# Optimization experiments

Measured on AMD Instinct MI355X. Metric: run time of the kernel, lower is better.

## Reference

```python
import jax, jax.numpy as jnp
import numpy as np

# Concrete instantiation of MACE MessagePassingConvolution for
# node irreps = 128x0e + 128x1o, target irreps = 128x0e + 128x1o, max_ell = 2.
# With these irreps the e3nn tensor product keeps exactly these paths:
#   0e (x) Y1o -> 1o ,  1o (x) Y1o -> 0e ,  1o (x) Y2e -> 1o
# plus the filtered original 0e and 1o features. Normalization constants are
# named below (stand-ins for e3nn's CG / component normalization).

C = 128                      # channels per irrep
AVG_NUM_NEIGHBORS = 10.0
SH_L1 = np.sqrt(3.0)         # component-normalized Y_1 scale
SH_L2 = np.sqrt(7.5)         # component-normalized Y_2 scale
CG_011 = 1.0 / np.sqrt(3.0)  # 0e x 1o -> 1o path norm
CG_110 = 1.0 / np.sqrt(3.0)  # 1o x 1o -> 0e path norm
CG_121 = np.sqrt(0.4)        # 1o x 2e -> 1o path norm


def setup_inputs() -> dict:
    key = jax.random.key(0)
    ks = jax.random.split(key, 9)
    N, E, R = 10000, 100000, 8
    return {
        "vectors": jax.random.normal(ks[0], (E, 3), jnp.float32),
        "node_feats": jax.random.normal(ks[1], (N, C + 3 * C), jnp.float32),
        "radial_embedding": jax.random.normal(ks[2], (E, R), jnp.float32),
        "w0": jax.random.normal(ks[3], (R, 64), jnp.float32),
        "w1": jax.random.normal(ks[4], (64, 64), jnp.float32),
        "w2": jax.random.normal(ks[5], (64, 64), jnp.float32),
        "w3": jax.random.normal(ks[6], (64, 5 * C), jnp.float32),
        "senders": jax.random.randint(ks[7], (E,), 0, N, jnp.int32),
        "receivers": jax.random.randint(ks[8], (E,), 0, N, jnp.int32),
    }


def reference(vectors, node_feats, radial_embedding, w0, w1, w2, w3, senders, receivers):
    N = node_feats.shape[0]
    s = node_feats[:, :C]                         # [N,C]   0e scalars
    v = node_feats[:, C:].reshape(N, C, 3)        # [N,C,3] 1o vectors

    # gather sender features onto edges
    ss = s[senders]                               # [E,C]
    vs = v[senders]                               # [E,C,3]

    # spherical harmonics of edge vectors (normalized input, per e3nn)
    rn = vectors / jnp.linalg.norm(vectors, axis=-1, keepdims=True)   # [E,3]
    Y1 = SH_L1 * rn                                                   # [E,3]  l=1
    Y2 = SH_L2 * (rn[:, :, None] * rn[:, None, :] - jnp.eye(3, dtype=rn.dtype) / 3.0)  # [E,3,3] l=2 (traceless sym)

    # tensor product paths filtered to target irreps 0e + 1o
    tp1 = CG_011 * ss[:, :, None] * Y1[:, None, :]            # [E,C,3]  0e x 1o -> 1o
    tp0 = CG_110 * jnp.einsum('eci,ei->ec', vs, Y1)           # [E,C]    1o x 1o -> 0e
    tp2 = CG_121 * jnp.einsum('eij,ecj->eci', Y2, vs)         # [E,C,3]  1o x 2e -> 1o

    # regrouped messages: scalars then vectors
    msg_s = jnp.concatenate([ss, tp0], axis=1)                # [E,2C]
    msg_v = jnp.concatenate([vs, tp1, tp2], axis=1)           # [E,3C,3]

    # radial MLP gating (e3nn-style normalized linears: x @ W / sqrt(fan_in))
    h = radial_embedding
    for W in (w0, w1, w2):
        h = jax.nn.silu(h @ W / jnp.sqrt(jnp.asarray(W.shape[0], h.dtype)))
    mix = h @ w3 / jnp.sqrt(jnp.asarray(w3.shape[0], h.dtype))        # [E,5C]

    msg_s = msg_s * mix[:, : 2 * C]
    msg_v = msg_v * mix[:, 2 * C :, None]

    # scatter-add into receivers, normalize by sqrt(avg_num_neighbors)
    out_s = jax.ops.segment_sum(msg_s, receivers, num_segments=N)     # [N,2C]
    out_v = jax.ops.segment_sum(msg_v, receivers, num_segments=N)     # [N,3C,3]
    out = jnp.concatenate([out_s, out_v.reshape(N, -1)], axis=1)      # [N,11C]
    return out / jnp.sqrt(jnp.asarray(AVG_NUM_NEIGHBORS, out.dtype))
```

## Files before the change

kernel.cpp:

```cpp
#include <hip/hip_runtime.h>

#define CCH   128
#define NF    512
#define OUTF  1408
#define RDIM  8

#define INV_SQRT8  0.35355339059327373f
#define INV_SQRT10 0.31622776601683794f
#define SQRT3      1.7320508075688772f

typedef _Float16 half2_t __attribute__((ext_vector_type(2)));

__device__ __forceinline__ float silu(float x) {
    return x / (1.0f + __expf(-x));
}

__device__ __forceinline__ unsigned int packh2(float lo, float hi) {
    half2_t h = { (_Float16)lo, (_Float16)hi };
    return __builtin_bit_cast(unsigned int, h);
}
__device__ __forceinline__ float h2lo(unsigned int u) {
    return (float)__builtin_bit_cast(half2_t, u).x;
}
__device__ __forceinline__ float h2hi(unsigned int u) {
    return (float)__builtin_bit_cast(half2_t, u).y;
}

__device__ __forceinline__ float dot2(unsigned int h, unsigned int w, float c) {
#if __has_builtin(__builtin_amdgcn_fdot2)
    return __builtin_amdgcn_fdot2(__builtin_bit_cast(half2_t, h),
                                  __builtin_bit_cast(half2_t, w), c, false);
#else
    half2_t a = __builtin_bit_cast(half2_t, h);
    half2_t b = __builtin_bit_cast(half2_t, w);
    return c + (float)a.x * (float)b.x + (float)a.y * (float)b.y;
#endif
}

__global__ void k_zero(int* __restrict__ p, int n) {
    int i = blockIdx.x * 256 + threadIdx.x;
    if (i < n) p[i] = 0;
}

__global__ void k_hist(const int* __restrict__ recv, int* __restrict__ counts, int E) {
    int i = blockIdx.x * 256 + threadIdx.x;
    if (i < E) atomicAdd(&counts[recv[i]], 1);
}

__global__ void k_scan(const int* __restrict__ counts, int* __restrict__ offsets,
                       int* __restrict__ cursor, int n) {
    __shared__ int wsum[16];
    int t = threadIdx.x;
    int lane = t & 63, wid = t >> 6;
    int carry = 0;
    for (int base = 0; base < n; base += 1024) {
        int i = base + t;
        int x = (i < n) ? counts[i] : 0;
        int s = x;
        #pragma unroll
        for (int off = 1; off < 64; off <<= 1) {
            int v = __shfl_up(s, off, 64);
            if (lane >= off) s += v;
        }
        if (lane == 63) wsum[wid] = s;
        __syncthreads();
        if (wid == 0) {
            int v = (lane < 16) ? wsum[lane] : 0;
            #pragma unroll
            for (int off = 1; off < 16; off <<= 1) {
                int u = __shfl_up(v, off, 64);
                if (lane >= off) v += u;
            }
            if (lane < 16) wsum[lane] = v;
        }
        __syncthreads();
        int excl_wave = (wid > 0) ? wsum[wid - 1] : 0;
        int incl = s + excl_wave;
        if (i < n) {
            int ex = carry + incl - x;
            offsets[i] = ex;
            cursor[i]  = ex;
        }
        carry += wsum[15];
        __syncthreads();
    }
    if (t == 0) offsets[n] = carry;
}

__global__ void k_perm(const int* __restrict__ recv, int* __restrict__ cursor,
                       int* __restrict__ perm, int E) {
    int i = blockIdx.x * 256 + threadIdx.x;
    if (i < E) {
        int p = atomicAdd(&cursor[recv[i]], 1);
        perm[p] = i;
    }
}

__global__ __launch_bounds__(256, 4) void k_mlp2(
    const float* __restrict__ radial,
    const float* __restrict__ w0, const float* __restrict__ w1,
    const float* __restrict__ w2, _Float16* __restrict__ h2out, int E)
{
    __shared__ float        w0s[8 * 64];
    __shared__ unsigned int w1p[32 * 64];
    __shared__ unsigned int w2p[32 * 64];
    __shared__ _Float16     hs[4][4][64];

    for (int idx = threadIdx.x; idx < 512; idx += 256) w0s[idx] = w0[idx];
    for (int idx = threadIdx.x; idx < 2048; idx += 256) {
        int j = idx & 63, kp = idx >> 6;
        w1p[idx] = packh2(w1[(2 * kp) * 64 + j], w1[(2 * kp + 1) * 64 + j]);
        w2p[idx] = packh2(w2[(2 * kp) * 64 + j], w2[(2 * kp + 1) * 64 + j]);
    }
    __syncthreads();

    const int lane = threadIdx.x & 63;
    const int wid  = threadIdx.x >> 6;
    unsigned int* hsu = (unsigned int*)&hs[wid][0][0];

    int e0 = (blockIdx.x * 4 + wid) * 4;

    float w0r[8];
    #pragma unroll
    for (int k = 0; k < 8; k++) w0r[k] = w0s[k * 64 + lane];
    #pragma unroll
    for (int q = 0; q < 4; q++) {
        int e = e0 + q; if (e >= E) e = E - 1;
        const float* r = radial + (size_t)e * RDIM;
        float acc = 0.f;
        #pragma unroll
        for (int k = 0; k < 8; k++) acc += r[k] * w0r[k];
        hs[wid][q][lane] = (_Float16)silu(acc * INV_SQRT8);
    }
    __syncthreads();

    float acc1[4] = {0.f, 0.f, 0.f, 0.f};
    #pragma unroll 4
    for (int kp = 0; kp < 32; kp++) {
        unsigned int w = w1p[kp * 64 + lane];
        #pragma unroll
        for (int q = 0; q < 4; q++) acc1[q] = dot2(hsu[q * 32 + kp], w, acc1[q]);
    }
    __syncthreads();
    #pragma unroll
    for (int q = 0; q < 4; q++) hs[wid][q][lane] = (_Float16)silu(acc1[q] * 0.125f);
    __syncthreads();

    float acc2[4] = {0.f, 0.f, 0.f, 0.f};
    #pragma unroll 4
    for (int kp = 0; kp < 32; kp++) {
        unsigned int w = w2p[kp * 64 + lane];
        #pragma unroll
        for (int q = 0; q < 4; q++) acc2[q] = dot2(hsu[q * 32 + kp], w, acc2[q]);
    }
    #pragma unroll
    for (int q = 0; q < 4; q++) {
        int e = e0 + q;
        if (e < E) h2out[(size_t)e * 64 + lane] = (_Float16)silu(acc2[q] * 0.125f);
    }
}

__global__ __launch_bounds__(512, 4) void k_mix(
    const float* __restrict__ w3,
    const unsigned int* __restrict__ h2g,
    unsigned int* __restrict__ mixp, int E)
{
    __shared__ uint4 wA[32 * 64];
    __shared__ uint4 wB[32 * 64];
    __shared__ uint2 wC[32 * 64];

    for (int idx = threadIdx.x; idx < 32 * 64; idx += 512) {
        int lane = idx & 63, kp = idx >> 6;
        const float* r0 = w3 + (2 * kp) * 640;
        const float* r1 = r0 + 640;
        uint4 A, B; uint2 Cc;
        A.x = packh2(r0[lane],       r1[lane]);
        A.y = packh2(r0[lane + 64],  r1[lane + 64]);
        A.z = packh2(r0[lane + 128], r1[lane + 128]);
        A.w = packh2(r0[lane + 192], r1[lane + 192]);
        B.x = packh2(r0[lane + 256], r1[lane + 256]);
        B.y = packh2(r0[lane + 320], r1[lane + 320]);
        B.z = packh2(r0[lane + 384], r1[lane + 384]);
        B.w = packh2(r0[lane + 448], r1[lane + 448]);
        Cc.x = packh2(r0[lane + 512], r1[lane + 512]);
        Cc.y = packh2(r0[lane + 576], r1[lane + 576]);
        wA[idx] = A; wB[idx] = B; wC[idx] = Cc;
    }
    __syncthreads();

    const int lane = threadIdx.x & 63;
    int wave = blockIdx.x * 8 + (threadIdx.x >> 6);
    int nwaves = gridDim.x * 8;
    int nquads = (E + 3) >> 2;
    const float sc = 0.125f * INV_SQRT10;

    for (int t = wave; t < nquads; t += nwaves) {
        int e0 = t * 4;
        const unsigned int* hp[4];
        #pragma unroll
        for (int q = 0; q < 4; q++) {
            int e = e0 + q; if (e >= E) e = E - 1;
            hp[q] = h2g + (size_t)e * 32;
        }

        float mixv[4][10];
        #pragma unroll
        for (int q = 0; q < 4; q++)
            #pragma unroll
            for (int m = 0; m < 10; m++) mixv[q][m] = 0.f;

        #pragma unroll 4
        for (int kp = 0; kp < 32; kp++) {
            unsigned int hq[4];
            #pragma unroll
            for (int q = 0; q < 4; q++) hq[q] = hp[q][kp];
            uint4 A  = wA[kp * 64 + lane];
            uint4 B  = wB[kp * 64 + lane];
            uint2 Cc = wC[kp * 64 + lane];
            #pragma unroll
            for (int q = 0; q < 4; q++) {
                unsigned int h = hq[q];
                mixv[q][0] = dot2(h, A.x,  mixv[q][0]);
                mixv[q][1] = dot2(h, A.y,  mixv[q][1]);
                mixv[q][2] = dot2(h, A.z,  mixv[q][2]);
                mixv[q][3] = dot2(h, A.w,  mixv[q][3]);
                mixv[q][4] = dot2(h, B.x,  mixv[q][4]);
                mixv[q][5] = dot2(h, B.y,  mixv[q][5]);
                mixv[q][6] = dot2(h, B.z,  mixv[q][6]);
                mixv[q][7] = dot2(h, B.w,  mixv[q][7]);
                mixv[q][8] = dot2(h, Cc.x, mixv[q][8]);
                mixv[q][9] = dot2(h, Cc.y, mixv[q][9]);
            }
        }

        #pragma unroll
        for (int q = 0; q < 4; q++) {
            int e = e0 + q;
            if (e < E) {
                unsigned int* mp = mixp + (size_t)e * 320 + lane;
                mp[0]   = packh2(mixv[q][0] * sc,         mixv[q][1] * sc);
                mp[64]  = packh2(mixv[q][2] * sc,         mixv[q][3] * sc);
                mp[128] = packh2(mixv[q][4] * sc,         mixv[q][5] * sc);
                mp[192] = packh2(mixv[q][6] * sc,         mixv[q][7] * sc);
                mp[256] = packh2(mixv[q][8] * sc * SQRT3, mixv[q][9] * sc * SQRT3);
            }
        }
    }
}

__global__ __launch_bounds__(256, 4) void k_gather(
    const float* __restrict__ vectors,
    const float* __restrict__ node_feats,
    const int*   __restrict__ senders,
    const int*   __restrict__ offsets,
    const int*   __restrict__ perm,
    const unsigned int* __restrict__ mixp,
    float* __restrict__ out, int N)
{
    const int lane = threadIdx.x & 63;
    int node = blockIdx.x * 4 + (threadIdx.x >> 6);
    if (node >= N) return;

    int beg = offsets[node];
    int end = offsets[node + 1];

    float aS[2]     = {0.f, 0.f};
    float aT0[2]    = {0.f, 0.f};
    float aV0[2][3] = {{0.f,0.f,0.f},{0.f,0.f,0.f}};
    float aV1[2][3] = {{0.f,0.f,0.f},{0.f,0.f,0.f}};
    float aV2[2][3] = {{0.f,0.f,0.f},{0.f,0.f,0.f}};

    for (int i = beg; i < end; i++) {
        int e = perm[i];
        float vx = vectors[(size_t)e * 3 + 0];
        float vy = vectors[(size_t)e * 3 + 1];
        float vz = vectors[(size_t)e * 3 + 2];
        float inv = rsqrtf(vx * vx + vy * vy + vz * vz);
        float rx = vx * inv, ry = vy * inv, rz = vz * inv;
        int snd = senders[e];

        const unsigned int* mp = mixp + (size_t)e * 320 + lane;
        unsigned int u0 = mp[0], u1 = mp[64], u2 = mp[128], u3 = mp[192], u4 = mp[256];

        const float* nf = node_feats + (size_t)snd * NF;
        #pragma unroll
        for (int t = 0; t < 2; t++) {
            int c = lane + 64 * t;
            float ssv = nf[c];
            float v0 = nf[CCH + 3 * c + 0];
            float v1 = nf[CCH + 3 * c + 1];
            float v2 = nf[CCH + 3 * c + 2];
            float d = rx * v0 + ry * v1 + rz * v2;

            float m0 = t ? h2hi(u0) : h2lo(u0);
            float m1 = t ? h2hi(u1) : h2lo(u1);
            float m2 = t ? h2hi(u2) : h2lo(u2);
            float m3 = t ? h2hi(u3) : h2lo(u3);
            float m4 = t ? h2hi(u4) : h2lo(u4);

            aS[t]  += ssv * m0;
            aT0[t] += d * m1;
            aV0[t][0] += v0 * m2;
            aV0[t][1] += v1 * m2;
            aV0[t][2] += v2 * m2;
            aV1[t][0] += ssv * rx * m3;
            aV1[t][1] += ssv * ry * m3;
            aV1[t][2] += ssv * rz * m3;
            aV2[t][0] += (d * rx - v0 * (1.f / 3.f)) * m4;
            aV2[t][1] += (d * ry - v1 * (1.f / 3.f)) * m4;
            aV2[t][2] += (d * rz - v2 * (1.f / 3.f)) * m4;
        }
    }

    float* ob = out + (size_t)node * OUTF;
    #pragma unroll
    for (int t = 0; t < 2; t++) {
        int c = lane + 64 * t;
        ob[c]                = aS[t];
        ob[CCH + c]          = aT0[t];
        ob[256  + 3 * c + 0] = aV0[t][0];
        ob[256  + 3 * c + 1] = aV0[t][1];
        ob[256  + 3 * c + 2] = aV0[t][2];
        ob[640  + 3 * c + 0] = aV1[t][0];
        ob[640  + 3 * c + 1] = aV1[t][1];
        ob[640  + 3 * c + 2] = aV1[t][2];
        ob[1024 + 3 * c + 0] = aV2[t][0];
        ob[1024 + 3 * c + 1] = aV2[t][1];
        ob[1024 + 3 * c + 2] = aV2[t][2];
    }
}

__global__ __launch_bounds__(512, 4) void k_main_fused(
    const float* __restrict__ vectors,
    const float* __restrict__ node_feats,
    const float* __restrict__ w3,
    const int*   __restrict__ senders,
    const int*   __restrict__ offsets,
    const int*   __restrict__ perm,
    const unsigned int* __restrict__ h2g,
    int* __restrict__ ctr,
    float* __restrict__ out, int N)
{
    __shared__ uint4 wA[32 * 64];
    __shared__ uint4 wB[32 * 64];
    __shared__ uint2 wC[32 * 64];

    for (int idx = threadIdx.x; idx < 32 * 64; idx += 512) {
        int lane = idx & 63, kp = idx >> 6;
        const float* r0 = w3 + (2 * kp) * 640;
        const float* r1 = r0 + 640;
        uint4 A, B; uint2 Cc;
        A.x = packh2(r0[lane],       r1[lane]);
        A.y = packh2(r0[lane + 64],  r1[lane + 64]);
        A.z = packh2(r0[lane + 128], r1[lane + 128]);
        A.w = packh2(r0[lane + 192], r1[lane + 192]);
        B.x = packh2(r0[lane + 256], r1[lane + 256]);
        B.y = packh2(r0[lane + 320], r1[lane + 320]);
        B.z = packh2(r0[lane + 384], r1[lane + 384]);
        B.w = packh2(r0[lane + 448], r1[lane + 448]);
        Cc.x = packh2(r0[lane + 512], r1[lane + 512]);
        Cc.y = packh2(r0[lane + 576], r1[lane + 576]);
        wA[idx] = A; wB[idx] = B; wC[idx] = Cc;
    }
    __syncthreads();

    const int lane = threadIdx.x & 63;

    while (true) {
        int t0 = 0;
        if (lane == 0) t0 = atomicAdd(ctr, 1);
        int node = __shfl(t0, 0, 64);
        if (node >= N) break;
        node = __builtin_amdgcn_readfirstlane(node);

        int beg = offsets[node];
        int end = offsets[node + 1];

        float aS[2]     = {0.f, 0.f};
        float aT0[2]    = {0.f, 0.f};
        float aV0[2][3] = {{0.f,0.f,0.f},{0.f,0.f,0.f}};
        float aV1[2][3] = {{0.f,0.f,0.f},{0.f,0.f,0.f}};
        float aV2[2][3] = {{0.f,0.f,0.f},{0.f,0.f,0.f}};

        for (int i0 = beg; i0 < end; i0 += 4) {
            int rem = end - i0;
            int nq = rem < 4 ? rem : 4;

            const unsigned int* hrow[4];
            float rnx[4], rny[4], rnz[4];
            int   snd[4];

            #pragma unroll
            for (int q = 0; q < 4; q++) {
                int e = (q < nq) ? perm[i0 + q] : perm[i0];
                e = __builtin_amdgcn_readfirstlane(e);
                hrow[q] = h2g + (size_t)e * 32;
                if (q < nq) {
                    float vx = vectors[(size_t)e * 3 + 0];
                    float vy = vectors[(size_t)e * 3 + 1];
                    float vz = vectors[(size_t)e * 3 + 2];
                    float inv = rsqrtf(vx * vx + vy * vy + vz * vz);
                    rnx[q] = vx * inv; rny[q] = vy * inv; rnz[q] = vz * inv;
                    snd[q] = senders[e];
                }
            }

            float mixv[4][10];
            #pragma unroll
            for (int q = 0; q < 4; q++)
                #pragma unroll
                for (int m = 0; m < 10; m++) mixv[q][m] = 0.f;

            #pragma unroll 4
            for (int kp = 0; kp < 32; kp++) {
                unsigned int hq[4];
                #pragma unroll
                for (int q = 0; q < 4; q++) hq[q] = hrow[q][kp];
                uint4 A  = wA[kp * 64 + lane];
                uint4 B  = wB[kp * 64 + lane];
                uint2 Cc = wC[kp * 64 + lane];
                #pragma unroll
                for (int q = 0; q < 4; q++) {
                    unsigned int h = hq[q];
                    mixv[q][0] = dot2(h, A.x,  mixv[q][0]);
                    mixv[q][1] = dot2(h, A.y,  mixv[q][1]);
                    mixv[q][2] = dot2(h, A.z,  mixv[q][2]);
                    mixv[q][3] = dot2(h, A.w,  mixv[q][3]);
                    mixv[q][4] = dot2(h, B.x,  mixv[q][4]);
                    mixv[q][5] = dot2(h, B.y,  mixv[q][5]);
                    mixv[q][6] = dot2(h, B.z,  mixv[q][6]);
                    mixv[q][7] = dot2(h, B.w,  mixv[q][7]);
                    mixv[q][8] = dot2(h, Cc.x, mixv[q][8]);
                    mixv[q][9] = dot2(h, Cc.y, mixv[q][9]);
                }
            }

            const float sc = 0.125f * INV_SQRT10;
            #pragma unroll
            for (int q = 0; q < 4; q++) {
                if (q < nq) {
                    const float* nf = node_feats + (size_t)snd[q] * NF;
                    #pragma unroll
                    for (int t = 0; t < 2; t++) {
                        int c = lane + 64 * t;
                        float ssv = nf[c];
                        float v0 = nf[CCH + 3 * c + 0];
                        float v1 = nf[CCH + 3 * c + 1];
                        float v2 = nf[CCH + 3 * c + 2];
                        float d = rnx[q] * v0 + rny[q] * v1 + rnz[q] * v2;

                        float m0 = mixv[q][t]     * sc;
                        float m1 = mixv[q][2 + t] * sc;
                        float m2 = mixv[q][4 + t] * sc;
                        float m3 = mixv[q][6 + t] * sc;
                        float m4 = mixv[q][8 + t] * sc * SQRT3;

                        aS[t]  += ssv * m0;
                        aT0[t] += d * m1;
                        aV0[t][0] += v0 * m2;
                        aV0[t][1] += v1 * m2;
                        aV0[t][2] += v2 * m2;
                        aV1[t][0] += ssv * rnx[q] * m3;
                        aV1[t][1] += ssv * rny[q] * m3;
                        aV1[t][2] += ssv * rnz[q] * m3;
                        aV2[t][0] += (d * rnx[q] - v0 * (1.f / 3.f)) * m4;
                        aV2[t][1] += (d * rny[q] - v1 * (1.f / 3.f)) * m4;
                        aV2[t][2] += (d * rnz[q] - v2 * (1.f / 3.f)) * m4;
                    }
                }
            }
        }

        float* ob = out + (size_t)node * OUTF;
        #pragma unroll
        for (int t = 0; t < 2; t++) {
            int c = lane + 64 * t;
            ob[c]                = aS[t];
            ob[CCH + c]          = aT0[t];
            ob[256  + 3 * c + 0] = aV0[t][0];
            ob[256  + 3 * c + 1] = aV0[t][1];
            ob[256  + 3 * c + 2] = aV0[t][2];
            ob[640  + 3 * c + 0] = aV1[t][0];
            ob[640  + 3 * c + 1] = aV1[t][1];
            ob[640  + 3 * c + 2] = aV1[t][2];
            ob[1024 + 3 * c + 0] = aV2[t][0];
            ob[1024 + 3 * c + 1] = aV2[t][1];
            ob[1024 + 3 * c + 2] = aV2[t][2];
        }
    }
}

extern "C" void kernel_launch(void* const* d_in, const int* in_sizes, int n_in,
                              void* d_out, int out_size, void* d_ws, size_t ws_size,
                              hipStream_t stream) {
    const float* vectors    = (const float*)d_in[0];
    const float* node_feats = (const float*)d_in[1];
    const float* radial     = (const float*)d_in[2];
    const float* w0         = (const float*)d_in[3];
    const float* w1         = (const float*)d_in[4];
    const float* w2         = (const float*)d_in[5];
    const float* w3         = (const float*)d_in[6];
    const int*   senders    = (const int*)d_in[7];
    const int*   receivers  = (const int*)d_in[8];

    int E = in_sizes[0] / 3;
    int N = in_sizes[1] / NF;

    size_t small_elems = (size_t)E * 32 + N + 1 + (N + 1) + N + E;
    size_t full_elems  = (size_t)E * 320 + small_elems;
    bool big = ws_size >= full_elems * 4;

    unsigned int* mixp = (unsigned int*)d_ws;
    unsigned int* h2u  = mixp + (big ? (size_t)E * 320 : 0);
    int* counts  = (int*)(h2u + (size_t)E * 32);
    int* ctr     = counts + N;
    int* offsets = ctr + 1;
    int* cursor  = offsets + N + 1;
    int* perm    = cursor + N;
    _Float16* h2f = (_Float16*)h2u;

    k_zero<<<(N + 1 + 255) / 256, 256, 0, stream>>>(counts, N + 1);
    k_hist<<<(E + 255) / 256, 256, 0, stream>>>(receivers, counts, E);
    k_scan<<<1, 1024, 0, stream>>>(counts, offsets, cursor, N);
    k_perm<<<(E + 255) / 256, 256, 0, stream>>>(receivers, cursor, perm, E);
    k_mlp2<<<(E + 15) / 16, 256, 0, stream>>>(radial, w0, w1, w2, h2f, E);

    if (big) {
        k_mix<<<512, 512, 0, stream>>>(w3, h2u, mixp, E);
        k_gather<<<(N + 3) / 4, 256, 0, stream>>>(vectors, node_feats, senders,
                                                  offsets, perm, mixp,
                                                  (float*)d_out, N);
    } else {
        k_main_fused<<<512, 512, 0, stream>>>(vectors, node_feats, w3, senders,
                                              offsets, perm, h2u, ctr,
                                              (float*)d_out, N);
    }
}
```

Baseline: 295.4 us.

## Use MFMA for radial mix matmul, persistent MLP blocks, two-edge gather batching

Replaces the dot2-based w3 projection with MFMA 16x16x32 f16 matrix instructions over 16-edge groups, staging w3 in a swizzled LDS layout to limit bank conflicts. The MLP kernel becomes grid-stride over a fixed 1024 blocks so the w1/w2 LDS packing is amortized across many edges. The gather loop handles two edges per iteration to overlap their loads, using float3 vector loads. The MFMA path depends on a correct operand layout and adds LDS swizzling complexity, and the output writes are now narrower and scattered.

```diff
diff --git a/kernel.cpp b/kernel.cpp
--- a/kernel.cpp
+++ b/kernel.cpp
@@ -10,6 +10,8 @@
 #define SQRT3      1.7320508075688772f
 
 typedef _Float16 half2_t __attribute__((ext_vector_type(2)));
+typedef _Float16 f16x8  __attribute__((ext_vector_type(8)));
+typedef float    f32x4  __attribute__((ext_vector_type(4)));
 
 __device__ __forceinline__ float silu(float x) {
     return x / (1.0f + __expf(-x));
@@ -118,131 +120,113 @@
     const int wid  = threadIdx.x >> 6;
     unsigned int* hsu = (unsigned int*)&hs[wid][0][0];
 
-    int e0 = (blockIdx.x * 4 + wid) * 4;
-
     float w0r[8];
     #pragma unroll
     for (int k = 0; k < 8; k++) w0r[k] = w0s[k * 64 + lane];
-    #pragma unroll
-    for (int q = 0; q < 4; q++) {
-        int e = e0 + q; if (e >= E) e = E - 1;
-        const float* r = radial + (size_t)e * RDIM;
-        float acc = 0.f;
-        #pragma unroll
-        for (int k = 0; k < 8; k++) acc += r[k] * w0r[k];
-        hs[wid][q][lane] = (_Float16)silu(acc * INV_SQRT8);
-    }
-    __syncthreads();
-
-    float acc1[4] = {0.f, 0.f, 0.f, 0.f};
-    #pragma unroll 4
-    for (int kp = 0; kp < 32; kp++) {
-        unsigned int w = w1p[kp * 64 + lane];
-        #pragma unroll
-        for (int q = 0; q < 4; q++) acc1[q] = dot2(hsu[q * 32 + kp], w, acc1[q]);
-    }
-    __syncthreads();
-    #pragma unroll
-    for (int q = 0; q < 4; q++) hs[wid][q][lane] = (_Float16)silu(acc1[q] * 0.125f);
-    __syncthreads();
-
-    float acc2[4] = {0.f, 0.f, 0.f, 0.f};
-    #pragma unroll 4
-    for (int kp = 0; kp < 32; kp++) {
-        unsigned int w = w2p[kp * 64 + lane];
-        #pragma unroll
-        for (int q = 0; q < 4; q++) acc2[q] = dot2(hsu[q * 32 + kp], w, acc2[q]);
-    }
-    #pragma unroll
-    for (int q = 0; q < 4; q++) {
-        int e = e0 + q;
-        if (e < E) h2out[(size_t)e * 64 + lane] = (_Float16)silu(acc2[q] * 0.125f);
-    }
-}
-
-__global__ __launch_bounds__(512, 4) void k_mix(
+
+    int nquads = (E + 3) >> 2;
+    for (int base = blockIdx.x * 4; base < nquads; base += gridDim.x * 4) {
+        int qd = base + wid;
+        bool active = qd < nquads;
+        int e0 = (active ? qd : nquads - 1) * 4;
+
+        #pragma unroll
+        for (int q = 0; q < 4; q++) {
+            int e = e0 + q; if (e >= E) e = E - 1;
+            const float* r = radial + (size_t)e * RDIM;
+            float acc = 0.f;
+            #pragma unroll
+            for (int k = 0; k < 8; k++) acc += r[k] * w0r[k];
+            hs[wid][q][lane] = (_Float16)silu(acc * INV_SQRT8);
+        }
+        __syncthreads();
+
+        float acc1[4] = {0.f, 0.f, 0.f, 0.f};
+        #pragma unroll 4
+        for (int kp = 0; kp < 32; kp++) {
+            unsigned int w = w1p[kp * 64 + lane];
+            #pragma unroll
+            for (int q = 0; q < 4; q++) acc1[q] = dot2(hsu[q * 32 + kp], w, acc1[q]);
+        }
+        __syncthreads();
+        #pragma unroll
+        for (int q = 0; q < 4; q++) hs[wid][q][lane] = (_Float16)silu(acc1[q] * 0.125f);
+        __syncthreads();
+
+        float acc2[4] = {0.f, 0.f, 0.f, 0.f};
+        #pragma unroll 4
+        for (int kp = 0; kp < 32; kp++) {
+            unsigned int w = w2p[kp * 64 + lane];
+            #pragma unroll
+            for (int q = 0; q < 4; q++) acc2[q] = dot2(hsu[q * 32 + kp], w, acc2[q]);
+        }
+        if (active) {
+            #pragma unroll
+            for (int q = 0; q < 4; q++) {
+                int e = e0 + q;
+                if (e < E) h2out[(size_t)e * 64 + lane] = (_Float16)silu(acc2[q] * 0.125f);
+            }
+        }
+        __syncthreads();
+    }
+}
+
+__global__ __launch_bounds__(512, 4) void k_mixm(
     const float* __restrict__ w3,
-    const unsigned int* __restrict__ h2g,
+    const unsigned int* __restrict__ h2u,
     unsigned int* __restrict__ mixp, int E)
 {
-    __shared__ uint4 wA[32 * 64];
-    __shared__ uint4 wB[32 * 64];
-    __shared__ uint2 wC[32 * 64];
-
-    for (int idx = threadIdx.x; idx < 32 * 64; idx += 512) {
-        int lane = idx & 63, kp = idx >> 6;
-        const float* r0 = w3 + (2 * kp) * 640;
-        const float* r1 = r0 + 640;
-        uint4 A, B; uint2 Cc;
-        A.x = packh2(r0[lane],       r1[lane]);
-        A.y = packh2(r0[lane + 64],  r1[lane + 64]);
-        A.z = packh2(r0[lane + 128], r1[lane + 128]);
-        A.w = packh2(r0[lane + 192], r1[lane + 192]);
-        B.x = packh2(r0[lane + 256], r1[lane + 256]);
-        B.y = packh2(r0[lane + 320], r1[lane + 320]);
-        B.z = packh2(r0[lane + 384], r1[lane + 384]);
-        B.w = packh2(r0[lane + 448], r1[lane + 448]);
-        Cc.x = packh2(r0[lane + 512], r1[lane + 512]);
-        Cc.y = packh2(r0[lane + 576], r1[lane + 576]);
-        wA[idx] = A; wB[idx] = B; wC[idx] = Cc;
+    __shared__ unsigned int ws3[640 * 32];
+
+    for (int idx = threadIdx.x; idx < 640 * 32; idx += 512) {
+        int n = idx >> 5, dw = idx & 31;
+        int q = dw >> 2, j = dw & 3;
+        int kb = q * 8 + 2 * j;
+        unsigned int val = packh2(w3[kb * 640 + n], w3[(kb + 1) * 640 + n]);
+        ws3[(n << 5) + (((q ^ (n & 7)) << 2) + j)] = val;
     }
     __syncthreads();
 
     const int lane = threadIdx.x & 63;
-    int wave = blockIdx.x * 8 + (threadIdx.x >> 6);
-    int nwaves = gridDim.x * 8;
-    int nquads = (E + 3) >> 2;
+    const int quad = lane >> 4, nl = lane & 15;
     const float sc = 0.125f * INV_SQRT10;
-
-    for (int t = wave; t < nquads; t += nwaves) {
-        int e0 = t * 4;
-        const unsigned int* hp[4];
-        #pragma unroll
-        for (int q = 0; q < 4; q++) {
-            int e = e0 + q; if (e >= E) e = E - 1;
-            hp[q] = h2g + (size_t)e * 32;
-        }
-
-        float mixv[4][10];
-        #pragma unroll
-        for (int q = 0; q < 4; q++)
-            #pragma unroll
-            for (int m = 0; m < 10; m++) mixv[q][m] = 0.f;
-
-        #pragma unroll 4
-        for (int kp = 0; kp < 32; kp++) {
-            unsigned int hq[4];
-            #pragma unroll
-            for (int q = 0; q < 4; q++) hq[q] = hp[q][kp];
-            uint4 A  = wA[kp * 64 + lane];
-            uint4 B  = wB[kp * 64 + lane];
-            uint2 Cc = wC[kp * 64 + lane];
-            #pragma unroll
-            for (int q = 0; q < 4; q++) {
-                unsigned int h = hq[q];
-                mixv[q][0] = dot2(h, A.x,  mixv[q][0]);
-                mixv[q][1] = dot2(h, A.y,  mixv[q][1]);
-                mixv[q][2] = dot2(h, A.z,  mixv[q][2]);
-                mixv[q][3] = dot2(h, A.w,  mixv[q][3]);
-                mixv[q][4] = dot2(h, B.x,  mixv[q][4]);
-                mixv[q][5] = dot2(h, B.y,  mixv[q][5]);
-                mixv[q][6] = dot2(h, B.z,  mixv[q][6]);
-                mixv[q][7] = dot2(h, B.w,  mixv[q][7]);
-                mixv[q][8] = dot2(h, Cc.x, mixv[q][8]);
-                mixv[q][9] = dot2(h, Cc.y, mixv[q][9]);
-            }
-        }
-
-        #pragma unroll
-        for (int q = 0; q < 4; q++) {
-            int e = e0 + q;
-            if (e < E) {
-                unsigned int* mp = mixp + (size_t)e * 320 + lane;
-                mp[0]   = packh2(mixv[q][0] * sc,         mixv[q][1] * sc);
-                mp[64]  = packh2(mixv[q][2] * sc,         mixv[q][3] * sc);
-                mp[128] = packh2(mixv[q][4] * sc,         mixv[q][5] * sc);
-                mp[192] = packh2(mixv[q][6] * sc,         mixv[q][7] * sc);
-                mp[256] = packh2(mixv[q][8] * sc * SQRT3, mixv[q][9] * sc * SQRT3);
+    int ngroups = (E + 15) >> 4;
+
+    for (int g = blockIdx.x * 8 + (threadIdx.x >> 6); g < ngroups; g += gridDim.x * 8) {
+        int eb = g << 4;
+        int erow = eb + nl; if (erow >= E) erow = E - 1;
+        const uint4* ha = (const uint4*)(h2u + (size_t)erow * 32);
+        f16x8 a0 = __builtin_bit_cast(f16x8, ha[quad]);
+        f16x8 a1 = __builtin_bit_cast(f16x8, ha[quad + 4]);
+
+        #pragma unroll
+        for (int mm = 0; mm < 5; mm++) {
+            f32x4 acc[8];
+            #pragma unroll
+            for (int t = 0; t < 8; t++) acc[t] = (f32x4){0.f, 0.f, 0.f, 0.f};
+
+            #pragma unroll
+            for (int t = 0; t < 8; t++) {
+                int nn = (mm * 8 + t) * 16 + nl;
+                const unsigned int* bp = ws3 + (nn << 5);
+                int sw = nn & 7;
+                f16x8 b0 = __builtin_bit_cast(f16x8, *(const uint4*)(bp + ((quad ^ sw) << 2)));
+                f16x8 b1 = __builtin_bit_cast(f16x8, *(const uint4*)(bp + (((quad + 4) ^ sw) << 2)));
+                acc[t] = __builtin_amdgcn_mfma_f32_16x16x32_f16(a0, b0, acc[t], 0, 0, 0);
+                acc[t] = __builtin_amdgcn_mfma_f32_16x16x32_f16(a1, b1, acc[t], 0, 0, 0);
+            }
+
+            float s = (mm == 4) ? sc * SQRT3 : sc;
+            #pragma unroll
+            for (int tp = 0; tp < 4; tp++) {
+                #pragma unroll
+                for (int r = 0; r < 4; r++) {
+                    int e = eb + quad * 4 + r;
+                    if (e < E) {
+                        mixp[(size_t)e * 320 + mm * 64 + tp * 16 + nl] =
+                            packh2(acc[tp][r] * s, acc[tp + 4][r] * s);
+                    }
+                }
             }
         }
     }
@@ -270,45 +254,59 @@
     float aV1[2][3] = {{0.f,0.f,0.f},{0.f,0.f,0.f}};
     float aV2[2][3] = {{0.f,0.f,0.f},{0.f,0.f,0.f}};
 
-    for (int i = beg; i < end; i++) {
-        int e = perm[i];
-        float vx = vectors[(size_t)e * 3 + 0];
-        float vy = vectors[(size_t)e * 3 + 1];
-        float vz = vectors[(size_t)e * 3 + 2];
-        float inv = rsqrtf(vx * vx + vy * vy + vz * vz);
-        float rx = vx * inv, ry = vy * inv, rz = vz * inv;
-        int snd = senders[e];
-
-        const unsigned int* mp = mixp + (size_t)e * 320 + lane;
-        unsigned int u0 = mp[0], u1 = mp[64], u2 = mp[128], u3 = mp[192], u4 = mp[256];
-
-        const float* nf = node_feats + (size_t)snd * NF;
-        #pragma unroll
-        for (int t = 0; t < 2; t++) {
-            int c = lane + 64 * t;
-            float ssv = nf[c];
-            float v0 = nf[CCH + 3 * c + 0];
-            float v1 = nf[CCH + 3 * c + 1];
-            float v2 = nf[CCH + 3 * c + 2];
-            float d = rx * v0 + ry * v1 + rz * v2;
-
-            float m0 = t ? h2hi(u0) : h2lo(u0);
-            float m1 = t ? h2hi(u1) : h2lo(u1);
-            float m2 = t ? h2hi(u2) : h2lo(u2);
-            float m3 = t ? h2hi(u3) : h2lo(u3);
-            float m4 = t ? h2hi(u4) : h2lo(u4);
-
-            aS[t]  += ssv * m0;
-            aT0[t] += d * m1;
-            aV0[t][0] += v0 * m2;
-            aV0[t][1] += v1 * m2;
-            aV0[t][2] += v2 * m2;
-            aV1[t][0] += ssv * rx * m3;
-            aV1[t][1] += ssv * ry * m3;
-            aV1[t][2] += ssv * rz * m3;
-            aV2[t][0] += (d * rx - v0 * (1.f / 3.f)) * m4;
-            aV2[t][1] += (d * ry - v1 * (1.f / 3.f)) * m4;
-            aV2[t][2] += (d * rz - v2 * (1.f / 3.f)) * m4;
+    for (int i = beg; i < end; i += 2) {
+        int cnt = end - i; if (cnt > 2) cnt = 2;
+        int ei[2];
+        ei[0] = perm[i];
+        ei[1] = (cnt == 2) ? perm[i + 1] : ei[0];
+
+        float3 ve[2];
+        const float* nfp[2];
+        unsigned int u[2][5];
+        #pragma unroll
+        for (int q = 0; q < 2; q++) {
+            int e = ei[q];
+            ve[q] = *(const float3*)(vectors + (size_t)e * 3);
+            nfp[q] = node_feats + (size_t)senders[e] * NF;
+            const unsigned int* mp = mixp + (size_t)e * 320 + lane;
+            #pragma unroll
+            for (int m = 0; m < 5; m++) u[q][m] = mp[m * 64];
+        }
+
+        #pragma unroll
+        for (int q = 0; q < 2; q++) {
+            if (q < cnt) {
+                float vx = ve[q].x, vy = ve[q].y, vz = ve[q].z;
+                float inv = rsqrtf(vx * vx + vy * vy + vz * vz);
+                float rx = vx * inv, ry = vy * inv, rz = vz * inv;
+                const float* nf = nfp[q];
+                #pragma unroll
+                for (int t = 0; t < 2; t++) {
+                    int c = lane + 64 * t;
+                    float ssv = nf[c];
+                    float3 vv = *(const float3*)(nf + CCH + 3 * c);
+                    float v0 = vv.x, v1 = vv.y, v2 = vv.z;
+                    float d = rx * v0 + ry * v1 + rz * v2;
+
+                    float m0 = t ? h2hi(u[q][0]) : h2lo(u[q][0]);
+                    float m1 = t ? h2hi(u[q][1]) : h2lo(u[q][1]);
+                    float m2 = t ? h2hi(u[q][2]) : h2lo(u[q][2]);
+                    float m3 = t ? h2hi(u[q][3]) : h2lo(u[q][3]);
+                    float m4 = t ? h2hi(u[q][4]) : h2lo(u[q][4]);
+
+                    aS[t]  += ssv * m0;
+                    aT0[t] += d * m1;
+                    aV0[t][0] += v0 * m2;
+                    aV0[t][1] += v1 * m2;
+                    aV0[t][2] += v2 * m2;
+                    aV1[t][0] += ssv * rx * m3;
+                    aV1[t][1] += ssv * ry * m3;
+                    aV1[t][2] += ssv * rz * m3;
+                    aV2[t][0] += (d * rx - v0 * (1.f / 3.f)) * m4;
+                    aV2[t][1] += (d * ry - v1 * (1.f / 3.f)) * m4;
+                    aV2[t][2] += (d * rz - v2 * (1.f / 3.f)) * m4;
+                }
+            }
         }
     }
 
@@ -523,10 +521,10 @@
     k_hist<<<(E + 255) / 256, 256, 0, stream>>>(receivers, counts, E);
     k_scan<<<1, 1024, 0, stream>>>(counts, offsets, cursor, N);
     k_perm<<<(E + 255) / 256, 256, 0, stream>>>(receivers, cursor, perm, E);
-    k_mlp2<<<(E + 15) / 16, 256, 0, stream>>>(radial, w0, w1, w2, h2f, E);
+    k_mlp2<<<1024, 256, 0, stream>>>(radial, w0, w1, w2, h2f, E);
 
     if (big) {
-        k_mix<<<512, 512, 0, stream>>>(w3, h2u, mixp, E);
+        k_mixm<<<512, 512, 0, stream>>>(w3, h2u, mixp, E);
         k_gather<<<(N + 3) / 4, 256, 0, stream>>>(vectors, node_feats, senders,
                                                   offsets, perm, mixp,
                                                   (float*)d_out, N);
```

New measurement: 449.1 us. 52.0% more time.
